# Performance work log

Hardware: AMD Instinct MI355X
Metric: run time of the kernel (lower is better)

Reference implementation:

```python
import jax, jax.numpy as jnp
import numpy as np

N, P, C, K = 16, 2048, 64, 16
EPS = 1e-5


def _bn(x, gamma, beta, axes):
    # training-mode batchnorm: biased variance over all dims except channel (last)
    m = jnp.mean(x, axis=axes, keepdims=True)
    v = jnp.var(x, axis=axes, keepdims=True)
    return (x - m) * jax.lax.rsqrt(v + EPS) * gamma + beta


def setup_inputs() -> dict:
    key = jax.random.key(0)
    ks = jax.random.split(key, 16)
    w = lambda k, shape: jax.random.normal(k, shape, jnp.float32) * 0.05
    inp = {"features": jax.random.normal(ks[0], (N, C, P), jnp.float32)}
    # edge-conv MLP: layer 0 takes 2*C input channels
    inp["w0"], inp["b0"] = w(ks[1], (C, 2 * C)), jnp.zeros((C,), jnp.float32)
    inp["g0"], inp["be0"] = jnp.ones((C,), jnp.float32), jnp.zeros((C,), jnp.float32)
    inp["w1"], inp["b1"] = w(ks[2], (C, C)), jnp.zeros((C,), jnp.float32)
    inp["g1"], inp["be1"] = jnp.ones((C,), jnp.float32), jnp.zeros((C,), jnp.float32)
    inp["w2"], inp["b2"] = w(ks[3], (C, C)), jnp.zeros((C,), jnp.float32)
    inp["g2"], inp["be2"] = jnp.ones((C,), jnp.float32), jnp.zeros((C,), jnp.float32)
    # shortcut 1x1 conv + BN
    inp["ws"], inp["bs"] = w(ks[4], (C, C)), jnp.zeros((C,), jnp.float32)
    inp["gs"], inp["bes"] = jnp.ones((C,), jnp.float32), jnp.zeros((C,), jnp.float32)
    return inp


def reference(features, w0, b0, g0, be0, w1, b1, g1, be1, w2, b2, g2, be2, ws, bs, gs, bes):
    # index != 0: features come in as (N, C, P) -> (N, P, C)
    X = jnp.transpose(features, (0, 2, 1))  # (N, P, C)

    # --- KNN via full pairwise squared distances ---
    r = jnp.sum(X * X, axis=-1)  # (N, P)
    d = r[:, :, None] - 2.0 * jnp.einsum('npc,nqc->npq', X, X) + r[:, None, :]
    _, idx = jax.lax.top_k(-d, K + 1)
    idx = idx[:, :, 1:]  # drop self, (N, P, K)

    # --- irregular gather + edge-feature concat ---
    f = X[jnp.arange(X.shape[0])[:, None, None], idx]  # (N, P, K, C)
    fc = jnp.broadcast_to(X[:, :, None, :], f.shape)   # center feature tiled
    h = jnp.concatenate([fc, fc - f], axis=-1)         # (N, P, K, 2C)

    def conv_bn_relu(h, w, b, g, be):
        h = jnp.einsum('npki,oi->npko', h, w) + b
        return jax.nn.relu(_bn(h, g, be, (0, 1, 2)))

    h = conv_bn_relu(h, w0, b0, g0, be0)
    h = conv_bn_relu(h, w1, b1, g1, be1)
    h = conv_bn_relu(h, w2, b2, g2, be2)
    h = jnp.mean(h, axis=2)  # aggregate over K -> (N, P, C)

    # shortcut: 1x1 conv + BN on center features
    sc = jnp.einsum('npi,oi->npo', X, ws) + bs
    sc = _bn(sc, gs, bes, (0, 1))

    out = jax.nn.relu(h + sc)           # (N, P, C)
    return jnp.transpose(out, (0, 2, 1))  # (N, C, P) to match torch layout
```

## Files before the change

### kernel.cpp

```cpp
#include <hip/hip_runtime.h>

using u16    = unsigned short;
using u64    = unsigned long long;
using bf16x8 = __attribute__((ext_vector_type(8))) short;
using f32x4  = __attribute__((ext_vector_type(4))) float;
using u16x4  = __attribute__((ext_vector_type(4))) u16;

#define NB   16
#define PP   2048
#define CC   64
#define KK   16
#define MROWS (NB*PP*KK)
#define NPTS  (NB*PP)

__device__ __forceinline__ float b2f(u16 u) { return __uint_as_float(((unsigned)u) << 16); }
__device__ __forceinline__ u16 f2b(float f) {
  unsigned u = __float_as_uint(f);
  return (u16)((u + 0x7fffu + ((u >> 16) & 1u)) >> 16);
}

__device__ __forceinline__ u64 dkey(float d, int qi) {
  unsigned u = __float_as_uint(d);
  u = u ^ (((unsigned)((int)u >> 31)) | 0x80000000u);
  return ((u64)u << 32) | (unsigned)qi;
}

template<bool UP>
__device__ __forceinline__ void ce(u64 &a, u64 &b) {
  const bool lt = a < b;
  const u64 lo = lt ? a : b;
  const u64 hi = lt ? b : a;
  if (UP) { a = lo; b = hi; } else { a = hi; b = lo; }
}

__device__ __forceinline__ void sort16(u64 (&v)[16]) {
  #pragma unroll
  for (int k = 2; k <= 16; k <<= 1) {
    #pragma unroll
    for (int j = k >> 1; j > 0; j >>= 1) {
      #pragma unroll
      for (int i = 0; i < 16; ++i) {
        const int l = i ^ j;
        if (l > i) {
          if ((i & k) == 0) ce<true>(v[i], v[l]);
          else              ce<false>(v[i], v[l]);
        }
      }
    }
  }
}

__device__ __forceinline__ void merge16(u64 (&dl)[16], const u64 (&nb)[16]) {
  u64 t[16];
  #pragma unroll
  for (int s = 0; s < 16; ++s) {
    const u64 a = dl[s], b = nb[15 - s];
    t[s] = a < b ? a : b;
  }
  #pragma unroll
  for (int j = 8; j > 0; j >>= 1) {
    #pragma unroll
    for (int i = 0; i < 16; ++i) {
      const int l = i ^ j;
      if (l > i) ce<true>(t[i], t[l]);
    }
  }
  #pragma unroll
  for (int s = 0; s < 16; ++s) dl[s] = t[s];
}

__global__ __launch_bounds__(256) void prep_k(const float* __restrict__ F,
                                              float* __restrict__ X,
                                              u16* __restrict__ Xb,
                                              float* __restrict__ r) {
  int gidx = blockIdx.x * 256 + threadIdx.x;
  int n = gidx >> 11, p = gidx & 2047;
  const float* src = F + (size_t)n * CC * PP + p;
  float v[CC];
  float rr = 0.f;
  #pragma unroll
  for (int c = 0; c < CC; ++c) { v[c] = src[(size_t)c * PP]; rr += v[c] * v[c]; }
  float* dst = X + (size_t)gidx * CC;
  #pragma unroll
  for (int c = 0; c < CC; c += 4) {
    float4 w; w.x = v[c]; w.y = v[c+1]; w.z = v[c+2]; w.w = v[c+3];
    *(float4*)(dst + c) = w;
  }
  u16* db = Xb + (size_t)gidx * CC;
  #pragma unroll
  for (int c = 0; c < CC; c += 8) {
    bf16x8 w8;
    #pragma unroll
    for (int j = 0; j < 8; ++j) w8[j] = (short)f2b(v[c + j]);
    *(bf16x8*)(db + c) = w8;
  }
  r[gidx] = rr;
}

__global__ __launch_bounds__(256) void cvtw_k(const float* __restrict__ w0, const float* __restrict__ w1,
                                              const float* __restrict__ w2, const float* __restrict__ wsb,
                                              u16* __restrict__ b0, u16* __restrict__ b1,
                                              u16* __restrict__ b2, u16* __restrict__ bs) {
  int i = blockIdx.x * 256 + threadIdx.x;
  if (i < 8192)        b0[i]          = f2b(w0[i]);
  else if (i < 12288)  b1[i - 8192]   = f2b(w1[i - 8192]);
  else if (i < 16384)  b2[i - 12288]  = f2b(w2[i - 12288]);
  else if (i < 20480)  bs[i - 16384]  = f2b(wsb[i - 16384]);
}

__global__ __launch_bounds__(512, 4)
void knn_k(const float* __restrict__ X,
           const float* __restrict__ r,
           u64* __restrict__ part) {
  __shared__ float lds[12800];
  float* Xp = lds;
  float* Xq = lds + 4352;

  const int n  = blockIdx.x >> 7;
  const int pb = ((blockIdx.x >> 2) & 31) * 64;
  const int qq = blockIdx.x & 3;
  const int qstart = qq * 512;
  const int t  = threadIdx.x;
  const float* Xn = X + (size_t)n * PP * CC;
  const float* rb = r + (size_t)n * PP;

  const int qh   = t & 31;
  const int pg   = t >> 5;
  const int prow = t & 63;
  const int w8   = t >> 6;
  const int u4   = (prow & 7) * 4;

  {
    const int pr = t & 63, ct = t >> 6;
    const float* src = Xn + (size_t)(pb + pr) * CC + ct * 8;
    #pragma unroll
    for (int j = 0; j < 8; j += 4) {
      float4 v = *(const float4*)(src + j);
      Xp[(ct*8 + j + 0) * 68 + pr] = v.x;
      Xp[(ct*8 + j + 1) * 68 + pr] = v.y;
      Xp[(ct*8 + j + 2) * 68 + pr] = v.z;
      Xp[(ct*8 + j + 3) * 68 + pr] = v.w;
    }
  }

  u64 dl[16];
  #pragma unroll
  for (int s = 0; s < 16; ++s) dl[s] = ~0ULL;

  #pragma unroll 1
  for (int qb = qstart; qb < qstart + 512; qb += 128) {
    __syncthreads();
    {
      const int qr = t & 127, hs = t >> 7;
      const float* src = Xn + (size_t)(qb + qr) * CC + hs * 16;
      #pragma unroll
      for (int j = 0; j < 16; j += 4) {
        float4 v = *(const float4*)(src + j);
        Xq[(hs*16 + j + 0) * 132 + qr] = v.x;
        Xq[(hs*16 + j + 1) * 132 + qr] = v.y;
        Xq[(hs*16 + j + 2) * 132 + qr] = v.z;
        Xq[(hs*16 + j + 3) * 132 + qr] = v.w;
      }
    }
    __syncthreads();

    float acc[4][4];
    #pragma unroll
    for (int i = 0; i < 4; ++i)
      #pragma unroll
      for (int j = 0; j < 4; ++j) acc[i][j] = 0.f;

    #pragma unroll 4
    for (int c = 0; c < 64; ++c) {
      const float4 a = *(const float4*)&Xp[c*68 + pg*4];
      const float4 bq = *(const float4*)&Xq[c*132 + qh*4];
      float av[4] = {a.x, a.y, a.z, a.w};
      float bv[4] = {bq.x, bq.y, bq.z, bq.w};
      #pragma unroll
      for (int i = 0; i < 4; ++i)
        #pragma unroll
        for (int j = 0; j < 4; ++j)
          acc[i][j] = fmaf(av[i], bv[j], acc[i][j]);
    }
    __syncthreads();

    {
      const int qg0 = qb + qh*4;
      const float4 rv = *(const float4*)(rb + qg0);
      #pragma unroll
      for (int i = 0; i < 4; ++i) {
        const int p  = pg*4 + i;
        const int pgl = pb + p;
        float d0 = rv.x - 2.f * acc[i][0]; if (qg0 + 0 == pgl) d0 = 3.0e38f;
        float d1 = rv.y - 2.f * acc[i][1]; if (qg0 + 1 == pgl) d1 = 3.0e38f;
        float d2 = rv.z - 2.f * acc[i][2]; if (qg0 + 2 == pgl) d2 = 3.0e38f;
        float d3 = rv.w - 2.f * acc[i][3]; if (qg0 + 3 == pgl) d3 = 3.0e38f;
        float4 dv; dv.x = d0; dv.y = d1; dv.z = d2; dv.w = d3;
        *(float4*)&Xq[(size_t)p * 132 + ((qh ^ ((p & 7) * 4)) * 4)] = dv;
      }
    }
    __syncthreads();

    {
      u64 nb[16];
      const float* drow = &Xq[(size_t)prow * 132];
      const int bbase = (w8 * 4) ^ u4;
      #pragma unroll
      for (int bb = 0; bb < 4; ++bb) {
        const float4 dv = *(const float4*)(drow + (bbase + bb) * 4);
        const int qg = qb + (w8*4 + bb) * 4;
        nb[bb*4+0] = dkey(dv.x, qg+0);
        nb[bb*4+1] = dkey(dv.y, qg+1);
        nb[bb*4+2] = dkey(dv.z, qg+2);
        nb[bb*4+3] = dkey(dv.w, qg+3);
      }
      sort16(nb);
      merge16(dl, nb);
    }
  }

  __syncthreads();
  {
    u64* mb = (u64*)lds;
    if (t >= 256) {
      #pragma unroll
      for (int s = 0; s < 16; ++s) mb[s * 256 + (t - 256)] = dl[s];
    }
    __syncthreads();
    if (t < 256) {
      u64 nb[16];
      #pragma unroll
      for (int s = 0; s < 16; ++s) nb[s] = mb[s * 256 + t];
      merge16(dl, nb);
    }
    __syncthreads();
    if (t < 256) {
      #pragma unroll
      for (int s = 0; s < 16; ++s) mb[s * 256 + t] = dl[s];
    }
    __syncthreads();
    if (t < 64) {
      #pragma unroll 1
      for (int j = 1; j < 4; ++j) {
        u64 nb[16];
        #pragma unroll
        for (int s = 0; s < 16; ++s) nb[s] = mb[s * 256 + (t + 64 * j)];
        merge16(dl, nb);
      }
      u64* outp = part + (((size_t)n * PP + pb + t) * 4 + qq) * 16;
      #pragma unroll
      for (int s = 0; s < 16; ++s) outp[s] = dl[s];
    }
  }
}

__global__ __launch_bounds__(256) void knnm_k(const u64* __restrict__ part,
                                              int* __restrict__ idx) {
  const int row = blockIdx.x * 256 + threadIdx.x;
  const u64* p = part + (size_t)row * 64;
  u64 dl[16];
  #pragma unroll
  for (int s = 0; s < 16; ++s) dl[s] = p[s];
  #pragma unroll 1
  for (int j = 1; j < 4; ++j) {
    u64 nb[16];
    #pragma unroll
    for (int s = 0; s < 16; ++s) nb[s] = p[j * 16 + s];
    merge16(dl, nb);
  }
  #pragma unroll
  for (int s = 0; s < 16; ++s)
    idx[(size_t)row * KK + s] = (int)(dl[s] & 0xFFFFFFFFu);
}

template<int KIN, bool GATHER, bool BNRELU>
__global__ __launch_bounds__(256) void conv_k(const u16* __restrict__ in,
                                              const int* __restrict__ idxp,
                                              const u16* __restrict__ wb,
                                              const float* __restrict__ bias,
                                              const float* __restrict__ st,
                                              u16* __restrict__ yout,
                                              float* __restrict__ partials) {
  constexpr int NKB = KIN / 32;
  __shared__ float sred[4][4][32];
  const int t = threadIdx.x;
  const int wv = t >> 6, l = t & 63, hi = l >> 4, lo = l & 15;
  const int rbase = blockIdx.x * 256 + wv * 64;

  bf16x8 wf[4][NKB];
  #pragma unroll
  for (int ob = 0; ob < 4; ++ob)
    #pragma unroll
    for (int kb = 0; kb < NKB; ++kb)
      wf[ob][kb] = *(const bf16x8*)(wb + (size_t)(ob*16 + lo) * KIN + kb*32 + hi*8);

  int qv[4];
  if constexpr (GATHER) {
    #pragma unroll
    for (int rb = 0; rb < 4; ++rb) {
      const int g = (rbase + rb*16) >> 4;
      qv[rb] = idxp[g * KK + lo];
    }
  }

  f32x4 acc[4][4];
  #pragma unroll
  for (int a = 0; a < 4; ++a)
    #pragma unroll
    for (int b = 0; b < 4; ++b) { f32x4 z = {0.f, 0.f, 0.f, 0.f}; acc[a][b] = z; }

  #pragma unroll
  for (int kb = 0; kb < NKB; ++kb) {
    float sv[8], tv[8];
    if constexpr (BNRELU) {
      const int k0 = kb*32 + hi*8;
      *(float4*)&sv[0] = *(const float4*)(st + k0);
      *(float4*)&sv[4] = *(const float4*)(st + k0 + 4);
      *(float4*)&tv[0] = *(const float4*)(st + KIN + k0);
      *(float4*)&tv[4] = *(const float4*)(st + KIN + k0 + 4);
    }
    bf16x8 af[4];
    #pragma unroll
    for (int rb = 0; rb < 4; ++rb) {
      if constexpr (GATHER) {
        const int g  = (rbase + rb*16) >> 4;
        const int k0 = kb*32 + hi*8;
        const bf16x8 fc = *(const bf16x8*)(in + (size_t)g * CC + (k0 & 63));
        if (kb < 2) {
          af[rb] = fc;
        } else {
          const int nn = g >> 11;
          const bf16x8 fv = *(const bf16x8*)(in + (size_t)(nn * PP + qv[rb]) * CC + (k0 & 63));
          bf16x8 df;
          #pragma unroll
          for (int j = 0; j < 8; ++j)
            df[j] = (short)f2b(b2f((u16)fc[j]) - b2f((u16)fv[j]));
          af[rb] = df;
        }
      } else {
        const int row = rbase + rb*16 + lo;
        const bf16x8 rv = *(const bf16x8*)(in + (size_t)row * KIN + kb*32 + hi*8);
        if constexpr (BNRELU) {
          bf16x8 tr;
          #pragma unroll
          for (int j = 0; j < 8; ++j) {
            const float x = fmaxf(b2f((u16)rv[j]) * sv[j] + tv[j], 0.f);
            tr[j] = (short)f2b(x);
          }
          af[rb] = tr;
        } else {
          af[rb] = rv;
        }
      }
    }
    #pragma unroll
    for (int ob = 0; ob < 4; ++ob)
      #pragma unroll
      for (int rb = 0; rb < 4; ++rb)
        acc[rb][ob] = __builtin_amdgcn_mfma_f32_16x16x32_bf16(wf[ob][kb], af[rb], acc[rb][ob], 0, 0, 0);
  }

  float ssum[16], qsum[16];
  #pragma unroll
  for (int j = 0; j < 16; ++j) { ssum[j] = 0.f; qsum[j] = 0.f; }
  #pragma unroll
  for (int ob = 0; ob < 4; ++ob) {
    const int o0 = ob*16 + hi*4;
    const float4 bv = *(const float4*)(bias + o0);
    #pragma unroll
    for (int rb = 0; rb < 4; ++rb) {
      const int row = rbase + rb*16 + lo;
      const float v0 = acc[rb][ob][0] + bv.x;
      const float v1 = acc[rb][ob][1] + bv.y;
      const float v2 = acc[rb][ob][2] + bv.z;
      const float v3 = acc[rb][ob][3] + bv.w;
      u16x4 pk; pk[0] = f2b(v0); pk[1] = f2b(v1); pk[2] = f2b(v2); pk[3] = f2b(v3);
      *(u16x4*)(yout + (size_t)row * CC + o0) = pk;
      ssum[ob*4+0] += v0; qsum[ob*4+0] += v0*v0;
      ssum[ob*4+1] += v1; qsum[ob*4+1] += v1*v1;
      ssum[ob*4+2] += v2; qsum[ob*4+2] += v2*v2;
      ssum[ob*4+3] += v3; qsum[ob*4+3] += v3*v3;
    }
  }
  #pragma unroll
  for (int m = 1; m < 16; m <<= 1) {
    #pragma unroll
    for (int j = 0; j < 16; ++j) {
      ssum[j] += __shfl_xor(ssum[j], m, 64);
      qsum[j] += __shfl_xor(qsum[j], m, 64);
    }
  }
  if (lo == 0) {
    #pragma unroll
    for (int j = 0; j < 16; ++j) {
      sred[wv][hi][j*2]   = ssum[j];
      sred[wv][hi][j*2+1] = qsum[j];
    }
  }
  __syncthreads();
  if (t < 128) {
    const int c = t & 63, half = t >> 6;
    const int slot = ((c >> 4) * 4 + (c & 3)) * 2 + half;
    const int h2 = (c >> 2) & 3;
    const float v = sred[0][h2][slot] + sred[1][h2][slot] + sred[2][h2][slot] + sred[3][h2][slot];
    partials[(size_t)blockIdx.x * 128 + half * 64 + c] = v;
  }
}

__global__ __launch_bounds__(256) void red1_k(const float* __restrict__ partials,
                                              float* __restrict__ out, int nwg) {
  __shared__ float accs[2][128];
  const int t = threadIdx.x, e = t & 127, h = t >> 7;
  float s = 0.f;
  for (int w = blockIdx.x + h * 64; w < nwg; w += 128)
    s += partials[(size_t)w * 128 + e];
  accs[h][e] = s;
  __syncthreads();
  if (t < 128) out[(size_t)blockIdx.x * 128 + t] = accs[0][t] + accs[1][t];
}

__global__ __launch_bounds__(128) void red2_k(const float* __restrict__ p2,
                                              const float* __restrict__ g,
                                              const float* __restrict__ be,
                                              float* __restrict__ st, float invM) {
  __shared__ float sq[128];
  const int t = threadIdx.x;
  float s = 0.f;
  #pragma unroll 8
  for (int w = 0; w < 64; ++w) s += p2[w * 128 + t];
  sq[t] = s;
  __syncthreads();
  if (t < 64) {
    const float S = sq[t], Q = sq[64 + t];
    const float m = S * invM;
    const float v = fmaxf(Q * invM - m * m, 0.f);
    const float sc = g[t] * rsqrtf(v + 1e-5f);
    st[t] = sc;
    st[64 + t] = be[t] - m * sc;
  }
}

__global__ __launch_bounds__(256) void final_k(const u16* __restrict__ y2,
                                               const u16* __restrict__ ysc,
                                               const float* __restrict__ st2,
                                               const float* __restrict__ stS,
                                               float* __restrict__ out) {
  __shared__ float ot[64][68];
  const int b = blockIdx.x, t = threadIdx.x;
  const int n = b >> 5, p0 = (b & 31) * 64;
  const int phh = t >> 2, jh = t & 3, c0 = jh * 16;
  const int g = n * PP + p0 + phh;
  float acc[16];
  #pragma unroll
  for (int i = 0; i < 16; ++i) acc[i] = 0.f;
  float sv[16], tv[16];
  #pragma unroll
  for (int i = 0; i < 16; ++i) { sv[i] = st2[c0 + i]; tv[i] = st2[64 + c0 + i]; }
  for (int k = 0; k < KK; ++k) {
    const u16* rp = y2 + ((size_t)g * KK + k) * CC + c0;
    const bf16x8 v0 = *(const bf16x8*)rp;
    const bf16x8 v1 = *(const bf16x8*)(rp + 8);
    #pragma unroll
    for (int j = 0; j < 8; ++j) {
      acc[j]     += fmaxf(b2f((u16)v0[j]) * sv[j]     + tv[j],     0.f);
      acc[8 + j] += fmaxf(b2f((u16)v1[j]) * sv[8 + j] + tv[8 + j], 0.f);
    }
  }
  const u16* sp = ysc + (size_t)g * CC + c0;
  const bf16x8 s0 = *(const bf16x8*)sp;
  const bf16x8 s1 = *(const bf16x8*)(sp + 8);
  #pragma unroll
  for (int i = 0; i < 16; ++i) {
    const float scx = b2f((u16)(i < 8 ? s0[i] : s1[i - 8])) * stS[c0 + i] + stS[64 + c0 + i];
    ot[c0 + i][phh] = fmaxf(acc[i] * (1.f / 16.f) + scx, 0.f);
  }
  __syncthreads();
  const int c = t >> 2, pc = t & 3;
  const float* src = &ot[c][pc * 16];
  float* dst = out + (size_t)n * CC * PP + (size_t)c * PP + p0 + pc * 16;
  #pragma unroll
  for (int j = 0; j < 16; j += 4) *(float4*)(dst + j) = *(const float4*)(src + j);
}

extern "C" void kernel_launch(void* const* d_in, const int* in_sizes, int n_in,
                              void* d_out, int out_size, void* d_ws, size_t ws_size,
                              hipStream_t stream) {
  (void)in_sizes; (void)n_in; (void)out_size; (void)ws_size;
  const float* F   = (const float*)d_in[0];
  const float* w0  = (const float*)d_in[1];
  const float* b0  = (const float*)d_in[2];
  const float* g0  = (const float*)d_in[3];
  const float* be0 = (const float*)d_in[4];
  const float* w1  = (const float*)d_in[5];
  const float* b1  = (const float*)d_in[6];
  const float* g1  = (const float*)d_in[7];
  const float* be1 = (const float*)d_in[8];
  const float* w2  = (const float*)d_in[9];
  const float* b2  = (const float*)d_in[10];
  const float* g2  = (const float*)d_in[11];
  const float* be2 = (const float*)d_in[12];
  const float* wS  = (const float*)d_in[13];
  const float* bS  = (const float*)d_in[14];
  const float* gS  = (const float*)d_in[15];
  const float* beS = (const float*)d_in[16];

  char* ws = (char*)d_ws;
  size_t off = 0;
  auto carve = [&](size_t bytes) -> void* {
    void* p = ws + off;
    off += (bytes + 255) & ~(size_t)255;
    return p;
  };
  float* X        = (float*)carve((size_t)NPTS * CC * 4);
  u16*   Xb       = (u16*)  carve((size_t)NPTS * CC * 2);
  float* rr       = (float*)carve((size_t)NPTS * 4);
  int*   idx      = (int*)  carve((size_t)NPTS * KK * 4);
  u16*   wb0      = (u16*)  carve(8192 * 2);
  u16*   wb1      = (u16*)  carve(4096 * 2);
  u16*   wb2      = (u16*)  carve(4096 * 2);
  u16*   wbs      = (u16*)  carve(4096 * 2);
  u16*   y        = (u16*)  carve((size_t)MROWS * CC * 2);
  u16*   ysc      = (u16*)  carve((size_t)NPTS * CC * 2);
  float* partials = (float*)carve((size_t)2048 * 128 * 4);
  float* p2       = (float*)carve((size_t)64 * 128 * 4);
  float* st0      = (float*)carve(128 * 4);
  float* st1      = (float*)carve(128 * 4);
  float* st2      = (float*)carve(128 * 4);
  float* stS      = (float*)carve(128 * 4);

  u64* part = (u64*)y;

  prep_k<<<NPTS / 256, 256, 0, stream>>>(F, X, Xb, rr);
  cvtw_k<<<80, 256, 0, stream>>>(w0, w1, w2, wS, wb0, wb1, wb2, wbs);
  knn_k<<<NB * 32 * 4, 512, 0, stream>>>(X, rr, part);
  knnm_k<<<NPTS / 256, 256, 0, stream>>>(part, idx);

  conv_k<128, true,  false><<<MROWS / 256, 256, 0, stream>>>(Xb, idx, wb0, b0, nullptr, y, partials);
  red1_k<<<64, 256, 0, stream>>>(partials, p2, MROWS / 256);
  red2_k<<<1, 128, 0, stream>>>(p2, g0, be0, st0, 1.f / (float)MROWS);

  conv_k<64, false, true><<<MROWS / 256, 256, 0, stream>>>(y, nullptr, wb1, b1, st0, y, partials);
  red1_k<<<64, 256, 0, stream>>>(partials, p2, MROWS / 256);
  red2_k<<<1, 128, 0, stream>>>(p2, g1, be1, st1, 1.f / (float)MROWS);

  conv_k<64, false, true><<<MROWS / 256, 256, 0, stream>>>(y, nullptr, wb2, b2, st1, y, partials);
  red1_k<<<64, 256, 0, stream>>>(partials, p2, MROWS / 256);
  red2_k<<<1, 128, 0, stream>>>(p2, g2, be2, st2, 1.f / (float)MROWS);

  conv_k<64, false, false><<<NPTS / 256, 256, 0, stream>>>(Xb, nullptr, wbs, bS, nullptr, ysc, partials);
  red1_k<<<64, 256, 0, stream>>>(partials, p2, NPTS / 256);
  red2_k<<<1, 128, 0, stream>>>(p2, gS, beS, stS, 1.f / (float)NPTS);

  final_k<<<NB * (PP / 64), 256, 0, stream>>>(y, ysc, st2, stS, (float*)d_out);
}
```

Before: 429.2 us.

## Compute KNN pairwise dot products with split-bf16 MFMA instead of FP32 FMA

The KNN distance Gram matrix moves from scalar FP32 FMAs to bf16 MFMA instructions. To keep near-FP32 accuracy, each feature is split into three bf16 terms (high, mid, low), and six cross-product MFMAs are accumulated per k-block. prep_k now writes these split bf16 arrays instead of an FP32 copy of X, and knn_k stages the bf16 tiles through 76.8KB of dynamic LDS. The trade-off is six times more matrix instructions and a larger LDS footprint, which may reduce occupancy. It also risks small numeric differences that could change neighbor ordering.

```diff
diff --git a/kernel.cpp b/kernel.cpp
--- a/kernel.cpp
+++ b/kernel.cpp
@@ -1,6 +1,7 @@
 #include <hip/hip_runtime.h>
 
 using u16    = unsigned short;
+using u32    = unsigned int;
 using u64    = unsigned long long;
 using bf16x8 = __attribute__((ext_vector_type(8))) short;
 using f32x4  = __attribute__((ext_vector_type(4))) float;
@@ -70,29 +71,35 @@
 }
 
 __global__ __launch_bounds__(256) void prep_k(const float* __restrict__ F,
-                                              float* __restrict__ X,
                                               u16* __restrict__ Xb,
+                                              u16* __restrict__ X3,
                                               float* __restrict__ r) {
   int gidx = blockIdx.x * 256 + threadIdx.x;
   int n = gidx >> 11, p = gidx & 2047;
   const float* src = F + (size_t)n * CC * PP + p;
-  float v[CC];
   float rr = 0.f;
-  #pragma unroll
-  for (int c = 0; c < CC; ++c) { v[c] = src[(size_t)c * PP]; rr += v[c] * v[c]; }
-  float* dst = X + (size_t)gidx * CC;
-  #pragma unroll
-  for (int c = 0; c < CC; c += 4) {
-    float4 w; w.x = v[c]; w.y = v[c+1]; w.z = v[c+2]; w.w = v[c+3];
-    *(float4*)(dst + c) = w;
+  u16 ha[CC], ma[CC], la[CC];
+  #pragma unroll
+  for (int c = 0; c < CC; ++c) {
+    const float x = src[(size_t)c * PP];
+    rr += x * x;
+    const u16 h = f2b(x);
+    const float eh = x - b2f(h);
+    const u16 m = f2b(eh);
+    const float el = eh - b2f(m);
+    const u16 lo_ = f2b(el);
+    ha[c] = h; ma[c] = m; la[c] = lo_;
   }
   u16* db = Xb + (size_t)gidx * CC;
+  u16* d3 = X3 + (size_t)gidx * 128;
   #pragma unroll
   for (int c = 0; c < CC; c += 8) {
-    bf16x8 w8;
-    #pragma unroll
-    for (int j = 0; j < 8; ++j) w8[j] = (short)f2b(v[c + j]);
-    *(bf16x8*)(db + c) = w8;
+    bf16x8 wh, wm, wl;
+    #pragma unroll
+    for (int j = 0; j < 8; ++j) { wh[j] = (short)ha[c+j]; wm[j] = (short)ma[c+j]; wl[j] = (short)la[c+j]; }
+    *(bf16x8*)(db + c)      = wh;
+    *(bf16x8*)(d3 + c)      = wm;
+    *(bf16x8*)(d3 + 64 + c) = wl;
   }
   r[gidx] = rr;
 }
@@ -109,38 +116,50 @@
 }
 
 __global__ __launch_bounds__(512, 4)
-void knn_k(const float* __restrict__ X,
-           const float* __restrict__ r,
-           u64* __restrict__ part) {
-  __shared__ float lds[12800];
-  float* Xp = lds;
-  float* Xq = lds + 4352;
+void knn_k(const u16* __restrict__ Xb, const u16* __restrict__ X3,
+           const float* __restrict__ r, u64* __restrict__ part) {
+  extern __shared__ char ldsraw[];
+  u16*   XpL = (u16*)ldsraw;
+  u16*   XqL = (u16*)(ldsraw + 25600);
+  float* D   = (float*)(ldsraw + 25600);
+  u64*   mb  = (u64*)ldsraw;
 
   const int n  = blockIdx.x >> 7;
   const int pb = ((blockIdx.x >> 2) & 31) * 64;
   const int qq = blockIdx.x & 3;
   const int qstart = qq * 512;
   const int t  = threadIdx.x;
-  const float* Xn = X + (size_t)n * PP * CC;
-  const float* rb = r + (size_t)n * PP;
-
-  const int qh   = t & 31;
-  const int pg   = t >> 5;
-  const int prow = t & 63;
-  const int w8   = t >> 6;
-  const int u4   = (prow & 7) * 4;
+  const int l  = t & 63, w = t >> 6;
+  const int P = w & 3, qhalf = w >> 2;
+  const int lo = l & 15, hi4 = l >> 4;
+
+  const u16*  Xbn = Xb + (size_t)(n * PP) * CC;
+  const u16*  X3n = X3 + (size_t)(n * PP) * 128;
+  const float* rb = r + n * PP;
 
   {
-    const int pr = t & 63, ct = t >> 6;
-    const float* src = Xn + (size_t)(pb + pr) * CC + ct * 8;
-    #pragma unroll
-    for (int j = 0; j < 8; j += 4) {
-      float4 v = *(const float4*)(src + j);
-      Xp[(ct*8 + j + 0) * 68 + pr] = v.x;
-      Xp[(ct*8 + j + 1) * 68 + pr] = v.y;
-      Xp[(ct*8 + j + 2) * 68 + pr] = v.z;
-      Xp[(ct*8 + j + 3) * 68 + pr] = v.w;
-    }
+    {
+      const int row = t >> 3, unit = t & 7;
+      *(bf16x8*)(XpL + row * 200 + unit * 8) =
+        *(const bf16x8*)(Xbn + (size_t)(pb + row) * CC + unit * 8);
+    }
+    #pragma unroll
+    for (int k = 0; k < 2; ++k) {
+      const int u = t + k * 512;
+      const int row = u >> 4, unit = u & 15;
+      *(bf16x8*)(XpL + row * 200 + 64 + unit * 8) =
+        *(const bf16x8*)(X3n + (size_t)(pb + row) * 128 + unit * 8);
+    }
+  }
+  __syncthreads();
+
+  bf16x8 ah[2], am[2], al[2];
+  #pragma unroll
+  for (int kb = 0; kb < 2; ++kb) {
+    const int base = (P * 16 + lo) * 200 + kb * 32 + hi4 * 8;
+    ah[kb] = *(const bf16x8*)(XpL + base);
+    am[kb] = *(const bf16x8*)(XpL + base + 64);
+    al[kb] = *(const bf16x8*)(XpL + base + 128);
   }
 
   u64 dl[16];
@@ -151,64 +170,75 @@
   for (int qb = qstart; qb < qstart + 512; qb += 128) {
     __syncthreads();
     {
-      const int qr = t & 127, hs = t >> 7;
-      const float* src = Xn + (size_t)(qb + qr) * CC + hs * 16;
-      #pragma unroll
-      for (int j = 0; j < 16; j += 4) {
-        float4 v = *(const float4*)(src + j);
-        Xq[(hs*16 + j + 0) * 132 + qr] = v.x;
-        Xq[(hs*16 + j + 1) * 132 + qr] = v.y;
-        Xq[(hs*16 + j + 2) * 132 + qr] = v.z;
-        Xq[(hs*16 + j + 3) * 132 + qr] = v.w;
-      }
-    }
-    __syncthreads();
-
-    float acc[4][4];
-    #pragma unroll
-    for (int i = 0; i < 4; ++i)
-      #pragma unroll
-      for (int j = 0; j < 4; ++j) acc[i][j] = 0.f;
-
-    #pragma unroll 4
-    for (int c = 0; c < 64; ++c) {
-      const float4 a = *(const float4*)&Xp[c*68 + pg*4];
-      const float4 bq = *(const float4*)&Xq[c*132 + qh*4];
-      float av[4] = {a.x, a.y, a.z, a.w};
-      float bv[4] = {bq.x, bq.y, bq.z, bq.w};
-      #pragma unroll
-      for (int i = 0; i < 4; ++i)
+      #pragma unroll
+      for (int k = 0; k < 2; ++k) {
+        const int u = t + k * 512;
+        const int row = u >> 3, unit = u & 7;
+        *(bf16x8*)(XqL + row * 200 + unit * 8) =
+          *(const bf16x8*)(Xbn + (size_t)(qb + row) * CC + unit * 8);
+      }
+      #pragma unroll
+      for (int k = 0; k < 4; ++k) {
+        const int u = t + k * 512;
+        const int row = u >> 4, unit = u & 15;
+        *(bf16x8*)(XqL + row * 200 + 64 + unit * 8) =
+          *(const bf16x8*)(X3n + (size_t)(qb + row) * 128 + unit * 8);
+      }
+    }
+    __syncthreads();
+
+    f32x4 acc[4];
+    #pragma unroll
+    for (int Q = 0; Q < 4; ++Q) { f32x4 z = {0.f, 0.f, 0.f, 0.f}; acc[Q] = z; }
+
+    #pragma unroll
+    for (int Q = 0; Q < 4; ++Q) {
+      const int qrow = qhalf * 64 + Q * 16 + lo;
+      #pragma unroll
+      for (int kb = 0; kb < 2; ++kb) {
+        const int base = qrow * 200 + kb * 32 + hi4 * 8;
+        const bf16x8 bh = *(const bf16x8*)(XqL + base);
+        const bf16x8 bm = *(const bf16x8*)(XqL + base + 64);
+        const bf16x8 bl = *(const bf16x8*)(XqL + base + 128);
+        acc[Q] = __builtin_amdgcn_mfma_f32_16x16x32_bf16(ah[kb], bh, acc[Q], 0, 0, 0);
+        acc[Q] = __builtin_amdgcn_mfma_f32_16x16x32_bf16(am[kb], bh, acc[Q], 0, 0, 0);
+        acc[Q] = __builtin_amdgcn_mfma_f32_16x16x32_bf16(ah[kb], bm, acc[Q], 0, 0, 0);
+        acc[Q] = __builtin_amdgcn_mfma_f32_16x16x32_bf16(al[kb], bh, acc[Q], 0, 0, 0);
+        acc[Q] = __builtin_amdgcn_mfma_f32_16x16x32_bf16(ah[kb], bl, acc[Q], 0, 0, 0);
+        acc[Q] = __builtin_amdgcn_mfma_f32_16x16x32_bf16(am[kb], bm, acc[Q], 0, 0, 0);
+      }
+    }
+    __syncthreads();
+
+    {
+      #pragma unroll
+      for (int Q = 0; Q < 4; ++Q) {
+        const int qloc  = qhalf * 64 + Q * 16 + lo;
+        const int qglob = qb + qloc;
+        const float rq  = rb[qglob];
+        const int bidx = qloc >> 2, qrem = qloc & 3;
         #pragma unroll
-        for (int j = 0; j < 4; ++j)
-          acc[i][j] = fmaf(av[i], bv[j], acc[i][j]);
-    }
-    __syncthreads();
-
-    {
-      const int qg0 = qb + qh*4;
-      const float4 rv = *(const float4*)(rb + qg0);
-      #pragma unroll
-      for (int i = 0; i < 4; ++i) {
-        const int p  = pg*4 + i;
-        const int pgl = pb + p;
-        float d0 = rv.x - 2.f * acc[i][0]; if (qg0 + 0 == pgl) d0 = 3.0e38f;
-        float d1 = rv.y - 2.f * acc[i][1]; if (qg0 + 1 == pgl) d1 = 3.0e38f;
-        float d2 = rv.z - 2.f * acc[i][2]; if (qg0 + 2 == pgl) d2 = 3.0e38f;
-        float d3 = rv.w - 2.f * acc[i][3]; if (qg0 + 3 == pgl) d3 = 3.0e38f;
-        float4 dv; dv.x = d0; dv.y = d1; dv.z = d2; dv.w = d3;
-        *(float4*)&Xq[(size_t)p * 132 + ((qh ^ ((p & 7) * 4)) * 4)] = dv;
+        for (int e = 0; e < 4; ++e) {
+          const int p = P * 16 + hi4 * 4 + e;
+          float d = rq - 2.f * acc[Q][e];
+          if (qglob == pb + p) d = 3.0e38f;
+          const int swz = ((bidx ^ ((p & 7) << 2)) << 2) + qrem;
+          D[p * 132 + swz] = d;
+        }
       }
     }
     __syncthreads();
 
     {
       u64 nb[16];
-      const float* drow = &Xq[(size_t)prow * 132];
-      const int bbase = (w8 * 4) ^ u4;
+      const int prow = l;
+      const float* drow = D + (size_t)prow * 132;
+      const int u4 = (prow & 7) * 4;
       #pragma unroll
       for (int bb = 0; bb < 4; ++bb) {
-        const float4 dv = *(const float4*)(drow + (bbase + bb) * 4);
-        const int qg = qb + (w8*4 + bb) * 4;
+        const int b = w * 4 + bb;
+        const float4 dv = *(const float4*)(drow + ((b ^ u4) * 4));
+        const int qg = qb + b * 4;
         nb[bb*4+0] = dkey(dv.x, qg+0);
         nb[bb*4+1] = dkey(dv.y, qg+1);
         nb[bb*4+2] = dkey(dv.z, qg+2);
@@ -221,7 +251,6 @@
 
   __syncthreads();
   {
-    u64* mb = (u64*)lds;
     if (t >= 256) {
       #pragma unroll
       for (int s = 0; s < 16; ++s) mb[s * 256 + (t - 256)] = dl[s];
@@ -511,8 +540,8 @@
     off += (bytes + 255) & ~(size_t)255;
     return p;
   };
-  float* X        = (float*)carve((size_t)NPTS * CC * 4);
   u16*   Xb       = (u16*)  carve((size_t)NPTS * CC * 2);
+  u16*   X3       = (u16*)  carve((size_t)NPTS * 128 * 2);
   float* rr       = (float*)carve((size_t)NPTS * 4);
   int*   idx      = (int*)  carve((size_t)NPTS * KK * 4);
   u16*   wb0      = (u16*)  carve(8192 * 2);
@@ -530,9 +559,9 @@
 
   u64* part = (u64*)y;
 
-  prep_k<<<NPTS / 256, 256, 0, stream>>>(F, X, Xb, rr);
+  prep_k<<<NPTS / 256, 256, 0, stream>>>(F, Xb, X3, rr);
   cvtw_k<<<80, 256, 0, stream>>>(w0, w1, w2, wS, wb0, wb1, wb2, wbs);
-  knn_k<<<NB * 32 * 4, 512, 0, stream>>>(X, rr, part);
+  knn_k<<<NB * 32 * 4, 512, 76800, stream>>>(Xb, X3, rr, part);
   knnm_k<<<NPTS / 256, 256, 0, stream>>>(part, idx);
 
   conv_k<128, true,  false><<<MROWS / 256, 256, 0, stream>>>(Xb, idx, wb0, b0, nullptr, y, partials);
```

Measured after the change: 495.8 us. 15.5% more time.
